# Optimization experiments

Hardware: AMD Instinct MI355X
Metric: run time of the kernel (lower is better)

The kernel has to match this reference:

```python
import jax, jax.numpy as jnp
import numpy as np

E = 1024  # embed_dim
H = 16    # num_heads
D = E // H
L = 2048  # seq len (Q_len == K_len == V_len)


def setup_inputs() -> dict:
    key = jax.random.key(0)
    ks = jax.random.split(key, 12)
    w = lambda k, shape: jax.random.normal(k, shape, dtype=jnp.float32) * 0.02
    return {
        "V": jax.random.normal(ks[0], (L, E), dtype=jnp.float32),
        "K": jax.random.normal(ks[1], (L, E), dtype=jnp.float32),
        "Q": jax.random.normal(ks[2], (L, E), dtype=jnp.float32),
        "position": jnp.arange(L, dtype=jnp.float32).reshape(1, L),
        "W_q": w(ks[3], (E, E)),
        "W_k": w(ks[4], (E, E)),
        "W_v": w(ks[5], (E, E)),
        "W_k_rel": w(ks[6], (E, 1)),
        "W_v_rel": w(ks[7], (E, 1)),
        "W_k_abs": w(ks[8], (E, 1)),
        "W_v_abs": w(ks[9], (E, 1)),
        "W_out": w(ks[10], (E, E)),
        "b_out": jnp.zeros((E,), dtype=jnp.float32),
    }


def reference(V, K, Q, position, W_q, W_k, W_v, W_k_rel, W_v_rel,
              W_k_abs, W_v_abs, W_out, b_out):
    pos = position[0]                                   # [L]
    q = (Q @ W_q.T).reshape(L, H, D)                    # [L,H,D]
    k = (K @ W_k.T).reshape(L, H, D)
    v = (V @ W_v.T).reshape(L, H, D)

    # Absolute position bias. NOTE: the original computes log(pos+1)/10 but then
    # overwrites it with the raw position (a bug preserved here faithfully):
    # Linear(1,E) on a scalar == scalar * weight vector.
    v = v + (pos[:, None] * W_v_abs[:, 0][None, :]).reshape(L, H, D)
    k = k + (pos[:, None] * W_k_abs[:, 0][None, :]).reshape(L, H, D)

    energy = jnp.einsum('qhd,khd->hqk', q, k)           # [H,L,L]

    # Relative-position K bias: relative_position_K[q,j,h,d] = rel[q,j] * wK[h,d]
    # so einsum('nqhd,nhqjd->nhqj') reduces exactly to rel[q,j] * (Q[q,h]\cdot wK[h]).
    rel = jnp.clip(jnp.abs(pos[:, None] - pos[None, :]), 0.0, 5000.0) / 5000.0  # [L,L]
    wK = W_k_rel[:, 0].reshape(H, D)
    wV = W_v_rel[:, 0].reshape(H, D)
    qw = jnp.einsum('qhd,hd->hq', q, wK)                # [H,L]
    energy = energy + qw[:, :, None] * rel[None]

    # Original scales by sqrt(embed_dim), not sqrt(head_dim).
    attn = jax.nn.softmax(energy / jnp.sqrt(jnp.float32(E)), axis=-1)  # [H,L,L]

    out = jnp.einsum('hqk,khd->qhd', attn, v)           # [L,H,D]
    # Relative-position V: sum_j attn[h,q,j]*rel[q,j]*wV[h,d] == (attn*rel summed over j) outer wV.
    s = jnp.einsum('hqk,qk->hq', attn, rel)             # [H,L]
    out = out + jnp.einsum('hq,hd->qhd', s, wV)

    return out.reshape(L, E) @ W_out.T + b_out          # [L,E]
```

## Files before the change

### kernel.cpp

```cpp
#include <hip/hip_runtime.h>
#include <stdint.h>

#define LL 2048
#define EE 1024
#define HH 16
#define DD 64
#define KX 1056

using short8 = __attribute__((ext_vector_type(8))) short;
using s4v    = __attribute__((ext_vector_type(4))) short;
using f32x4  = __attribute__((ext_vector_type(4))) float;

#if __has_builtin(__builtin_amdgcn_mfma_f32_16x16x16_bf16)
#define MFMA16(a,b,c) __builtin_amdgcn_mfma_f32_16x16x16_bf16(a,b,c,0,0,0)
#elif __has_builtin(__builtin_amdgcn_mfma_f32_16x16x16bf16_1k)
#define MFMA16(a,b,c) __builtin_amdgcn_mfma_f32_16x16x16bf16_1k(a,b,c,0,0,0)
#else
static __device__ __forceinline__ f32x4 mfma16f(s4v a, s4v b, f32x4 c) {
  asm volatile("v_mfma_f32_16x16x16_bf16 %0, %1, %2, %0" : "+v"(c) : "v"(a), "v"(b));
  return c;
}
#define MFMA16(a,b,c) mfma16f(a,b,c)
#endif

__device__ __forceinline__ short f2bf(float x) {
  union { float f; uint32_t u; } v; v.f = x;
  uint32_t r = v.u + 0x7fffu + ((v.u >> 16) & 1u);
  return (short)(r >> 16);
}

__global__ __launch_bounds__(256) void convall(
    const float* __restrict__ Q, const float* __restrict__ K,
    const float* __restrict__ V, const float* __restrict__ Wq,
    const float* __restrict__ Wk, const float* __restrict__ Wv,
    const float* __restrict__ Wout,
    short* __restrict__ Qb, short* __restrict__ Kb, short* __restrict__ Vb,
    short* __restrict__ Wqb, short* __restrict__ Wkb, short* __restrict__ Wvb,
    short* __restrict__ W2) {
  const int S1 = LL * EE / 4;
  const int SW = EE * EE / 4;
  int i4 = blockIdx.x * 256 + threadIdx.x;
  const float* src; short* dst; int idx4; bool strided = false;
  if (i4 < 3 * S1) {
    int z = i4 >> 19; idx4 = i4 & (S1 - 1);
    src = z == 0 ? Q : (z == 1 ? K : V);
    dst = z == 0 ? Qb : (z == 1 ? Kb : Vb);
  } else {
    int j = i4 - 3 * S1;
    int z = j >> 18; idx4 = j & (SW - 1);
    src = z == 0 ? Wq : (z == 1 ? Wk : (z == 2 ? Wv : Wout));
    dst = z == 0 ? Wqb : (z == 1 ? Wkb : (z == 2 ? Wvb : W2));
    strided = (z == 3);
  }
  int i = idx4 * 4;
  const float4 v = *(const float4*)(src + i);
  int di = strided ? ((i >> 10) * KX + (i & 1023)) : i;
  union { short s[4]; uint64_t u; } p;
  p.s[0] = f2bf(v.x); p.s[1] = f2bf(v.y); p.s[2] = f2bf(v.z); p.s[3] = f2bf(v.w);
  *(uint64_t*)(dst + di) = p.u;
}

__global__ __launch_bounds__(256) void uker(const float* __restrict__ Wq,
                                            const float* __restrict__ wabs,
                                            const float* __restrict__ wrel,
                                            float* __restrict__ u) {
  int flat = blockIdx.x * 256 + threadIdx.x;
  int c = flat & (EE - 1);
  int h = (flat >> 10) & (HH - 1);
  int s = flat >> 14;
  const float* w = s ? wrel : wabs;
  float acc = 0.f;
  #pragma unroll 8
  for (int d = 0; d < DD; ++d)
    acc += Wq[(size_t)(h * DD + d) * EE + c] * w[h * DD + d];
  u[flat] = acc;
}

__global__ __launch_bounds__(256) void qawker(const float* __restrict__ Q,
                                              const float* __restrict__ u,
                                              float* __restrict__ qaw) {
  int i = blockIdx.x;
  int t = threadIdx.x;
  int h = t >> 4, seg = t & 15;
  const float* u0 = u + (size_t)h * EE;
  const float* u1 = u + (size_t)HH * EE + (size_t)h * EE;
  const float* q = Q + (size_t)i * EE;
  float a0 = 0.f, a1 = 0.f;
  for (int cc = 0; cc < 64; ++cc) {
    int c = cc * 16 + seg;
    float qv = q[c];
    a0 += qv * u0[c];
    a1 += qv * u1[c];
  }
  #pragma unroll
  for (int m = 1; m < 16; m <<= 1) {
    a0 += __shfl_xor(a0, m);
    a1 += __shfl_xor(a1, m);
  }
  if (seg == 0) { qaw[i * 32 + h] = a0; qaw[i * 32 + 16 + h] = a1; }
}

__global__ __launch_bounds__(256) void mrelker(const float* __restrict__ Wout,
                                               const float* __restrict__ wva,
                                               const float* __restrict__ wvr,
                                               short* __restrict__ W2) {
  int flat = blockIdx.x * 256 + threadIdx.x;
  int n = flat >> 5;
  int s = (flat >> 4) & 1;
  int h = flat & 15;
  const float* w = s ? wvr : wva;
  float acc = 0.f;
  #pragma unroll 8
  for (int d = 0; d < DD; ++d)
    acc += Wout[(size_t)n * EE + h * DD + d] * w[h * DD + d];
  W2[(size_t)n * KX + 1024 + s * 16 + h] = f2bf(acc);
}

__global__ __launch_bounds__(256) void gemm_bt(
    const short* __restrict__ Aall, const short* __restrict__ Ball,
    void* __restrict__ Call,
    int K, int aBatch, int bBatch, int cBatch,
    int ldc, int vTransZ, int ldcT, int bf16Out,
    const float* __restrict__ bias, int scaleZ, float scaleVal)
{
  const int BM = 64, BN = 128, BK = 32, PAD = 8;
  __shared__ short As[BM][BK + PAD];
  __shared__ short Bs[BN][BK + PAD];
  int z = blockIdx.z;
  const short* A = Aall + (size_t)z * aBatch;
  const short* B = Ball + (size_t)z * bBatch;
  int m0 = blockIdx.y * BM, n0 = blockIdx.x * BN;
  int t = threadIdx.x;
  int lane = t & 63, wave = t >> 6;
  int wm = wave >> 1, wn = wave & 1;
  int fr = lane & 15, fo = (lane >> 4) * 8;
  const f32x4 vzero = {0.f, 0.f, 0.f, 0.f};
  f32x4 acc[2][4];
  #pragma unroll
  for (int i = 0; i < 2; ++i)
    #pragma unroll
    for (int j = 0; j < 4; ++j) acc[i][j] = vzero;

  int kTiles = K / BK;
  for (int kt = 0; kt < kTiles; ++kt) {
    __syncthreads();
    {
      int row = t >> 2, kb = (t & 3) * 8;
      *(short8*)&As[row][kb] =
          *(const short8*)(A + (size_t)(m0 + row) * K + kt * BK + kb);
      *(short8*)&Bs[row][kb] =
          *(const short8*)(B + (size_t)(n0 + row) * K + kt * BK + kb);
      int uu = t + 256;
      int row2 = uu >> 2, kb2 = (uu & 3) * 8;
      *(short8*)&Bs[row2][kb2] =
          *(const short8*)(B + (size_t)(n0 + row2) * K + kt * BK + kb2);
    }
    __syncthreads();
    short8 af[2], bfr[4];
    #pragma unroll
    for (int i = 0; i < 2; ++i) af[i] = *(const short8*)&As[wm * 32 + i * 16 + fr][fo];
    #pragma unroll
    for (int j = 0; j < 4; ++j) bfr[j] = *(const short8*)&Bs[wn * 64 + j * 16 + fr][fo];
    #pragma unroll
    for (int i = 0; i < 2; ++i)
      #pragma unroll
      for (int j = 0; j < 4; ++j)
        acc[i][j] = __builtin_amdgcn_mfma_f32_16x16x32_bf16(af[i], bfr[j], acc[i][j], 0, 0, 0);
  }

  int rb = (lane >> 4) * 4;
  bool doTrans = (z == vTransZ);
  bool doScale = (z == scaleZ);
  #pragma unroll
  for (int i = 0; i < 2; ++i) {
    #pragma unroll
    for (int j = 0; j < 4; ++j) {
      int n = n0 + wn * 64 + j * 16 + fr;
      float bv = bias ? bias[n] : 0.f;
      #pragma unroll
      for (int r = 0; r < 4; ++r) {
        int m = m0 + wm * 32 + i * 16 + rb + r;
        float val = acc[i][j][r];
        if (doScale) val *= scaleVal;
        val += bv;
        if (bf16Out) {
          short* C = (short*)Call + (size_t)z * cBatch;
          if (doTrans) C[(size_t)n * ldcT + m] = f2bf(val);
          else         C[(size_t)m * ldc + n] = f2bf(val);
        } else {
          float* C = (float*)Call;
          C[(size_t)m * ldc + n] = val;
        }
      }
    }
  }
}

__global__ __launch_bounds__(256, 4) void flash2(
    const short* __restrict__ qp, const short* __restrict__ kp,
    const short* __restrict__ vpT, const float* __restrict__ qaw,
    float* __restrict__ Opart, float* __restrict__ stats)
{
  const int KB = 64;
  __shared__ short k_lds[64][72];
  __shared__ short v_lds[64][72];
  int h = blockIdx.y;
  int q0 = blockIdx.x * 64;
  int half = blockIdx.z;
  int kbeg = half * 1024;
  int t = threadIdx.x, w = t >> 6, lane = t & 63;
  int g = lane >> 4, fr = lane & 15;
  int gi = q0 + w * 16 + fr;
  float gif = (float)gi;
  const f32x4 vzero = {0.f, 0.f, 0.f, 0.f};

  short8 qf[2];
  #pragma unroll
  for (int ks = 0; ks < 2; ++ks)
    qf[ks] = *(const short8*)(qp + (size_t)gi * EE + h * 64 + ks * 32 + g * 8);

  const float LOG2E = 1.4426950408889634f;
  const float sc = LOG2E / 32.f;
  float qa_s = qaw[gi * 32 + h] * sc;
  float qw_s = qaw[gi * 32 + 16 + h] * (sc / 5000.f);

  float m2 = -1e30f, lsum = 0.f, SpA = 0.f, SrA = 0.f;
  f32x4 Oa[4];
  #pragma unroll
  for (int fc = 0; fc < 4; ++fc) Oa[fc] = vzero;

  for (int kt = 0; kt < 16; ++kt) {
    int k0 = kbeg + kt * KB;
    __syncthreads();
    #pragma unroll
    for (int uu = 0; uu < 2; ++uu) {
      int u2 = t + uu * 256;
      int row = u2 >> 3, cb = (u2 & 7) * 8;
      *(short8*)&k_lds[row][cb] =
          *(const short8*)(kp + (size_t)(k0 + row) * EE + h * 64 + cb);
      *(short8*)&v_lds[row][cb] =
          *(const short8*)(vpT + (size_t)(h * 64 + row) * LL + k0 + cb);
    }
    __syncthreads();

    f32x4 St[4];
    #pragma unroll
    for (int jt = 0; jt < 4; ++jt) {
      f32x4 a = vzero;
      a = __builtin_amdgcn_mfma_f32_16x16x32_bf16(
              *(const short8*)&k_lds[jt * 16 + fr][g * 8], qf[0], a, 0, 0, 0);
      a = __builtin_amdgcn_mfma_f32_16x16x32_bf16(
              *(const short8*)&k_lds[jt * 16 + fr][32 + g * 8], qf[1], a, 0, 0, 0);
      St[jt] = a;
    }

    float pf[4][4];
    float tm = -1e30f;
    #pragma unroll
    for (int jt = 0; jt < 4; ++jt) {
      float jb = (float)(k0 + jt * 16 + 4 * g);
      #pragma unroll
      for (int r = 0; r < 4; ++r) {
        float jgf = jb + (float)r;
        float e = St[jt][r] + jgf * qa_s + fabsf(gif - jgf) * qw_s;
        pf[jt][r] = e;
        tm = fmaxf(tm, e);
      }
    }
    tm = fmaxf(tm, __shfl_xor(tm, 16));
    tm = fmaxf(tm, __shfl_xor(tm, 32));

    if (__any(tm > m2 + 8.f)) {
      float mn = fmaxf(m2, tm);
      float alpha = exp2f(m2 - mn);
      m2 = mn;
      lsum *= alpha; SpA *= alpha; SrA *= alpha;
      #pragma unroll
      for (int r = 0; r < 4; ++r) {
        float alr = __shfl(alpha, ((lane >> 4) << 2) + r);
        #pragma unroll
        for (int fc = 0; fc < 4; ++fc) Oa[fc][r] *= alr;
      }
    }

    float Pt = 0.f, Spt = 0.f;
    #pragma unroll
    for (int jt = 0; jt < 4; ++jt) {
      float jb = (float)(k0 + jt * 16 + 4 * g);
      #pragma unroll
      for (int r = 0; r < 4; ++r) {
        float p = exp2f(pf[jt][r] - m2);
        pf[jt][r] = p;
        Pt += p;
        Spt = fmaf(p, jb + (float)r, Spt);
      }
    }
    lsum += Pt; SpA += Spt;
    if (gi >= k0 + KB)      SrA += gif * Pt - Spt;
    else if (gi < k0)       SrA += Spt - gif * Pt;
    else {
      #pragma unroll
      for (int jt = 0; jt < 4; ++jt) {
        float jb = (float)(k0 + jt * 16 + 4 * g);
        #pragma unroll
        for (int r = 0; r < 4; ++r)
          SrA += pf[jt][r] * fabsf(gif - (jb + (float)r));
      }
    }

    s4v pa[4];
    #pragma unroll
    for (int jt = 0; jt < 4; ++jt) {
      int lo, hi;
      asm("v_cvt_pk_bf16_f32 %0, %1, %2" : "=v"(lo) : "v"(pf[jt][0]), "v"(pf[jt][1]));
      asm("v_cvt_pk_bf16_f32 %0, %1, %2" : "=v"(hi) : "v"(pf[jt][2]), "v"(pf[jt][3]));
      union { int i[2]; s4v s; } uu; uu.i[0] = lo; uu.i[1] = hi;
      pa[jt] = uu.s;
    }

    #pragma unroll
    for (int jt = 0; jt < 4; ++jt) {
      #pragma unroll
      for (int fc = 0; fc < 4; ++fc) {
        s4v vb = *(const s4v*)&v_lds[fc * 16 + fr][jt * 16 + 4 * g];
        Oa[fc] = MFMA16(pa[jt], vb, Oa[fc]);
      }
    }
  }

  lsum += __shfl_xor(lsum, 16); lsum += __shfl_xor(lsum, 32);
  SpA  += __shfl_xor(SpA, 16);  SpA  += __shfl_xor(SpA, 32);
  SrA  += __shfl_xor(SrA, 16);  SrA  += __shfl_xor(SrA, 32);

  size_t sb = (size_t)(half * HH + h) * LL;
  if (g == 0) {
    float4 s4 = {m2, lsum, SpA, SrA};
    *(float4*)&stats[(sb + q0 + w * 16 + fr) * 4] = s4;
  }
  #pragma unroll
  for (int fc = 0; fc < 4; ++fc)
    #pragma unroll
    for (int r = 0; r < 4; ++r)
      Opart[(sb + q0 + w * 16 + 4 * g + r) * 64 + fc * 16 + fr] = Oa[fc][r];
}

__global__ __launch_bounds__(256) void merge(const float* __restrict__ Opart,
                                             const float* __restrict__ stats,
                                             short* __restrict__ X2) {
  int q = blockIdx.x;
  int t = threadIdx.x;
  int h = t >> 4, ds = (t & 15) * 4;
  const float4 s0 = *(const float4*)&stats[((size_t)h * LL + q) * 4];
  const float4 s1 = *(const float4*)&stats[((size_t)(HH + h) * LL + q) * 4];
  float m = fmaxf(s0.x, s1.x);
  float a0 = exp2f(s0.x - m), a1 = exp2f(s1.x - m);
  float inv = 1.f / (s0.y * a0 + s1.y * a1);
  const float4 O0 = *(const float4*)&Opart[((size_t)h * LL + q) * 64 + ds];
  const float4 O1 = *(const float4*)&Opart[((size_t)(HH + h) * LL + q) * 64 + ds];
  union { short s[4]; uint64_t u; } pk;
  pk.s[0] = f2bf((O0.x * a0 + O1.x * a1) * inv);
  pk.s[1] = f2bf((O0.y * a0 + O1.y * a1) * inv);
  pk.s[2] = f2bf((O0.z * a0 + O1.z * a1) * inv);
  pk.s[3] = f2bf((O0.w * a0 + O1.w * a1) * inv);
  *(uint64_t*)&X2[(size_t)q * KX + h * 64 + ds] = pk.u;
  if (t < 32) {
    int hh = t & 15;
    const float4 t0 = *(const float4*)&stats[((size_t)hh * LL + q) * 4];
    const float4 t1 = *(const float4*)&stats[((size_t)(HH + hh) * LL + q) * 4];
    float mm = fmaxf(t0.x, t1.x);
    float b0 = exp2f(t0.x - mm), b1 = exp2f(t1.x - mm);
    float linv = 1.f / (t0.y * b0 + t1.y * b1);
    float val = (t < 16) ? (t0.z * b0 + t1.z * b1) * linv
                         : (t0.w * b0 + t1.w * b1) * linv * (1.f / 5000.f);
    X2[(size_t)q * KX + 1024 + (t < 16 ? hh : 16 + hh)] = f2bf(val);
  }
}

extern "C" void kernel_launch(void* const* d_in, const int* in_sizes, int n_in,
                              void* d_out, int out_size, void* d_ws, size_t ws_size,
                              hipStream_t stream) {
  const float* V    = (const float*)d_in[0];
  const float* Kin  = (const float*)d_in[1];
  const float* Q    = (const float*)d_in[2];
  const float* Wq   = (const float*)d_in[4];
  const float* Wk   = (const float*)d_in[5];
  const float* Wv   = (const float*)d_in[6];
  const float* Wkr  = (const float*)d_in[7];
  const float* Wvr  = (const float*)d_in[8];
  const float* Wka  = (const float*)d_in[9];
  const float* Wva  = (const float*)d_in[10];
  const float* Wout = (const float*)d_in[11];
  const float* bout = (const float*)d_in[12];

  char* ws = (char*)d_ws;
  size_t off = 0;
  auto alloc = [&](size_t bytes) -> void* {
    void* p = ws + off;
    off = (off + bytes + 255) & ~(size_t)255;
    return p;
  };
  short* Qb  = (short*)alloc((size_t)LL * EE * 2);
  short* Kb  = (short*)alloc((size_t)LL * EE * 2);
  short* Vb  = (short*)alloc((size_t)LL * EE * 2);
  short* Wqb = (short*)alloc((size_t)EE * EE * 2);
  short* Wkb = (short*)alloc((size_t)EE * EE * 2);
  short* Wvb = (short*)alloc((size_t)EE * EE * 2);
  short* qp  = (short*)alloc((size_t)LL * EE * 2);
  short* kp  = (short*)alloc((size_t)LL * EE * 2);
  short* vpT = (short*)alloc((size_t)EE * LL * 2);
  short* W2  = (short*)alloc((size_t)EE * KX * 2);
  short* X2  = (short*)alloc((size_t)LL * KX * 2);
  float* u   = (float*)alloc((size_t)2 * HH * EE * 4);
  float* qaw = (float*)alloc((size_t)LL * 32 * 4);
  float* Opart = (float*)Qb;
  float* stats = (float*)((char*)Qb + (size_t)17 * 1024 * 1024);
  (void)in_sizes; (void)n_in; (void)out_size; (void)ws_size;

  const float sc = 1.4426950408889634f / 32.f;

  convall<<<(3 * LL * EE / 4 + 4 * EE * EE / 4) / 256, 256, 0, stream>>>(
      Q, Kin, V, Wq, Wk, Wv, Wout, Qb, Kb, Vb, Wqb, Wkb, Wvb, W2);

  uker<<<(2 * HH * EE) / 256, 256, 0, stream>>>(Wq, Wka, Wkr, u);
  qawker<<<LL, 256, 0, stream>>>(Q, u, qaw);
  mrelker<<<(EE * 32) / 256, 256, 0, stream>>>(Wout, Wva, Wvr, W2);

  dim3 gp(EE / 128, LL / 64, 3);
  gemm_bt<<<gp, 256, 0, stream>>>(Qb, Wqb, qp, EE,
                                  LL * EE, EE * EE, LL * EE,
                                  EE, 2, LL, 1,
                                  nullptr, 0, sc);

  flash2<<<dim3(LL / 64, HH, 2), 256, 0, stream>>>(qp, kp, vpT, qaw, Opart, stats);

  merge<<<LL, 256, 0, stream>>>(Opart, stats, X2);

  dim3 go(EE / 128, LL / 64, 1);
  gemm_bt<<<go, 256, 0, stream>>>(X2, W2, d_out, KX,
                                  0, 0, 0,
                                  EE, -1, 1, 0,
                                  bout, -1, 1.f);
}
```

Before: 155.1 us.

## Split attention keys four ways and fold row statistics into an extra MFMA tile

The flash kernel now splits the key range into four chunks instead of two, doubling the grid. The per-element position bias is rewritten as precomputed per-lane offsets plus a per-tile constant for off-diagonal tiles. The row sums (P, P·j, masked sums) are computed by a fifth MFMA column block over synthetic V rows instead of scalar reductions. Partial outputs are normalised and stored as bf16, halving the partial-output traffic, and the merge kernel combines four splits. This adds LDS setup and bf16 rounding of the partials, and relies on bf16-encoded key indices being exact.

```diff
diff --git a/kernel.cpp b/kernel.cpp
--- a/kernel.cpp
+++ b/kernel.cpp
@@ -27,6 +27,10 @@
   union { float f; uint32_t u; } v; v.f = x;
   uint32_t r = v.u + 0x7fffu + ((v.u >> 16) & 1u);
   return (short)(r >> 16);
+}
+__device__ __forceinline__ float bf2f(short s) {
+  union { uint32_t u; float f; } v; v.u = ((uint32_t)(uint16_t)s) << 16;
+  return v.f;
 }
 
 __global__ __launch_bounds__(256) void convall(
@@ -196,24 +200,26 @@
   }
 }
 
-__global__ __launch_bounds__(256, 4) void flash2(
+__global__ __launch_bounds__(256, 4) void flash3(
     const short* __restrict__ qp, const short* __restrict__ kp,
     const short* __restrict__ vpT, const float* __restrict__ qaw,
-    float* __restrict__ Opart, float* __restrict__ stats)
+    short* __restrict__ Obf, float* __restrict__ stats)
 {
-  const int KB = 64;
-  __shared__ short k_lds[64][72];
-  __shared__ short v_lds[64][72];
+  __shared__ __align__(16) short k_lds[64][68];
+  __shared__ __align__(16) short v_lds[80][68];
   int h = blockIdx.y;
   int q0 = blockIdx.x * 64;
-  int half = blockIdx.z;
-  int kbeg = half * 1024;
+  int split = blockIdx.z;
+  int kbeg = split * 512;
   int t = threadIdx.x, w = t >> 6, lane = t & 63;
   int g = lane >> 4, fr = lane & 15;
   int gi = q0 + w * 16 + fr;
   float gif = (float)gi;
   const f32x4 vzero = {0.f, 0.f, 0.f, 0.f};
 
+  if (t < 64) v_lds[65][t] = (short)0x3F80;
+  if (t < 204) ((uint64_t*)&v_lds[68][0])[t] = 0ull;
+
   short8 qf[2];
   #pragma unroll
   for (int ks = 0; ks < 2; ++ks)
@@ -224,13 +230,23 @@
   float qa_s = qaw[gi * 32 + h] * sc;
   float qw_s = qaw[gi * 32 + 16 + h] * (sc / 5000.f);
 
-  float m2 = -1e30f, lsum = 0.f, SpA = 0.f, SrA = 0.f;
-  f32x4 Oa[4];
-  #pragma unroll
-  for (int fc = 0; fc < 4; ++fc) Oa[fc] = vzero;
-
-  for (int kt = 0; kt < 16; ++kt) {
-    int k0 = kbeg + kt * KB;
+  float jp_[16], jm_[16];
+  #pragma unroll
+  for (int jt = 0; jt < 4; ++jt)
+    #pragma unroll
+    for (int r = 0; r < 4; ++r) {
+      float jl = (float)(jt * 16 + 4 * g + r);
+      jp_[jt * 4 + r] = jl * (qa_s + qw_s);
+      jm_[jt * 4 + r] = jl * (qa_s - qw_s);
+    }
+
+  float m2 = -1e30f, Ptd = 0.f, Sptd = 0.f, Srtd = 0.f;
+  f32x4 Oa[5];
+  #pragma unroll
+  for (int fc = 0; fc < 5; ++fc) Oa[fc] = vzero;
+
+  for (int kt = 0; kt < 8; ++kt) {
+    int k0 = kbeg + kt * 64;
     __syncthreads();
     #pragma unroll
     for (int uu = 0; uu < 2; ++uu) {
@@ -241,6 +257,13 @@
       *(short8*)&v_lds[row][cb] =
           *(const short8*)(vpT + (size_t)(h * 64 + row) * LL + k0 + cb);
     }
+    if (t < 64) {
+      short jv = f2bf((float)(k0 - kbeg + t));
+      bool after = (k0 > q0);
+      v_lds[64][t] = jv;
+      v_lds[66][t] = after ? jv : (short)0;
+      v_lds[67][t] = after ? (short)0x3F80 : (short)0;
+    }
     __syncthreads();
 
     f32x4 St[4];
@@ -255,57 +278,73 @@
     }
 
     float pf[4][4];
-    float tm = -1e30f;
-    #pragma unroll
-    for (int jt = 0; jt < 4; ++jt) {
-      float jb = (float)(k0 + jt * 16 + 4 * g);
-      #pragma unroll
-      for (int r = 0; r < 4; ++r) {
-        float jgf = jb + (float)r;
-        float e = St[jt][r] + jgf * qa_s + fabsf(gif - jgf) * qw_s;
-        pf[jt][r] = e;
-        tm = fmaxf(tm, e);
-      }
-    }
-    tm = fmaxf(tm, __shfl_xor(tm, 16));
-    tm = fmaxf(tm, __shfl_xor(tm, 32));
-
-    if (__any(tm > m2 + 8.f)) {
-      float mn = fmaxf(m2, tm);
+    float tmv = -1e30f, C;
+    if (k0 < q0) {
+      C = k0 * qa_s + (gif - (float)k0) * qw_s;
+      #pragma unroll
+      for (int jt = 0; jt < 4; ++jt)
+        #pragma unroll
+        for (int r = 0; r < 4; ++r) {
+          float e = St[jt][r] + jm_[jt * 4 + r];
+          pf[jt][r] = e;
+          tmv = fmaxf(tmv, e);
+        }
+    } else if (k0 > q0) {
+      C = k0 * qa_s + ((float)k0 - gif) * qw_s;
+      #pragma unroll
+      for (int jt = 0; jt < 4; ++jt)
+        #pragma unroll
+        for (int r = 0; r < 4; ++r) {
+          float e = St[jt][r] + jp_[jt * 4 + r];
+          pf[jt][r] = e;
+          tmv = fmaxf(tmv, e);
+        }
+    } else {
+      C = 0.f;
+      #pragma unroll
+      for (int jt = 0; jt < 4; ++jt)
+        #pragma unroll
+        for (int r = 0; r < 4; ++r) {
+          float jgf = (float)(k0 + jt * 16 + 4 * g + r);
+          float e = St[jt][r] + jgf * qa_s + fabsf(gif - jgf) * qw_s;
+          pf[jt][r] = e;
+          tmv = fmaxf(tmv, e);
+        }
+    }
+    tmv = fmaxf(tmv, __shfl_xor(tmv, 16));
+    tmv = fmaxf(tmv, __shfl_xor(tmv, 32));
+    float tmt = tmv + C;
+
+    if (__any(tmt > m2 + 8.f)) {
+      float mn = fmaxf(m2, tmt);
       float alpha = exp2f(m2 - mn);
       m2 = mn;
-      lsum *= alpha; SpA *= alpha; SrA *= alpha;
+      Ptd *= alpha; Sptd *= alpha; Srtd *= alpha;
       #pragma unroll
       for (int r = 0; r < 4; ++r) {
         float alr = __shfl(alpha, ((lane >> 4) << 2) + r);
         #pragma unroll
-        for (int fc = 0; fc < 4; ++fc) Oa[fc][r] *= alr;
+        for (int fc = 0; fc < 5; ++fc) Oa[fc][r] *= alr;
       }
     }
-
-    float Pt = 0.f, Spt = 0.f;
-    #pragma unroll
-    for (int jt = 0; jt < 4; ++jt) {
-      float jb = (float)(k0 + jt * 16 + 4 * g);
-      #pragma unroll
-      for (int r = 0; r < 4; ++r) {
-        float p = exp2f(pf[jt][r] - m2);
-        pf[jt][r] = p;
-        Pt += p;
-        Spt = fmaf(p, jb + (float)r, Spt);
-      }
-    }
-    lsum += Pt; SpA += Spt;
-    if (gi >= k0 + KB)      SrA += gif * Pt - Spt;
-    else if (gi < k0)       SrA += Spt - gif * Pt;
-    else {
-      #pragma unroll
-      for (int jt = 0; jt < 4; ++jt) {
-        float jb = (float)(k0 + jt * 16 + 4 * g);
+    float mr = m2 - C;
+    #pragma unroll
+    for (int jt = 0; jt < 4; ++jt)
+      #pragma unroll
+      for (int r = 0; r < 4; ++r)
+        pf[jt][r] = exp2f(pf[jt][r] - mr);
+
+    if (k0 == q0) {
+      #pragma unroll
+      for (int jt = 0; jt < 4; ++jt)
         #pragma unroll
-        for (int r = 0; r < 4; ++r)
-          SrA += pf[jt][r] * fabsf(gif - (jb + (float)r));
-      }
+        for (int r = 0; r < 4; ++r) {
+          float jgf = (float)(k0 + jt * 16 + 4 * g + r);
+          float p = pf[jt][r];
+          Ptd += p;
+          Sptd = fmaf(p, jgf, Sptd);
+          Srtd = fmaf(p, fabsf(gif - jgf), Srtd);
+        }
     }
 
     s4v pa[4];
@@ -321,57 +360,102 @@
     #pragma unroll
     for (int jt = 0; jt < 4; ++jt) {
       #pragma unroll
-      for (int fc = 0; fc < 4; ++fc) {
+      for (int fc = 0; fc < 5; ++fc) {
         s4v vb = *(const s4v*)&v_lds[fc * 16 + fr][jt * 16 + 4 * g];
         Oa[fc] = MFMA16(pa[jt], vb, Oa[fc]);
       }
     }
   }
 
-  lsum += __shfl_xor(lsum, 16); lsum += __shfl_xor(lsum, 32);
-  SpA  += __shfl_xor(SpA, 16);  SpA  += __shfl_xor(SpA, 32);
-  SrA  += __shfl_xor(SrA, 16);  SrA  += __shfl_xor(SrA, 32);
-
-  size_t sb = (size_t)(half * HH + h) * LL;
+  Ptd  += __shfl_xor(Ptd, 16);  Ptd  += __shfl_xor(Ptd, 32);
+  Sptd += __shfl_xor(Sptd, 16); Sptd += __shfl_xor(Sptd, 32);
+  Srtd += __shfl_xor(Srtd, 16); Srtd += __shfl_xor(Srtd, 32);
+
+  __syncthreads();
+  float* scr = (float*)&k_lds[0][0];
+  if (fr < 4) {
+    #pragma unroll
+    for (int r = 0; r < 4; ++r)
+      scr[(w * 16 + 4 * g + r) * 4 + fr] = Oa[4][r];
+  }
+  __syncthreads();
+
+  float inv[4];
+  #pragma unroll
+  for (int r = 0; r < 4; ++r)
+    inv[r] = 1.f / scr[(w * 16 + 4 * g + r) * 4 + 1];
+
   if (g == 0) {
-    float4 s4 = {m2, lsum, SpA, SrA};
-    *(float4*)&stats[(sb + q0 + w * 16 + fr) * 4] = s4;
-  }
+    float e0 = scr[(w * 16 + fr) * 4 + 0];
+    float e1 = scr[(w * 16 + fr) * 4 + 1];
+    float e2 = scr[(w * 16 + fr) * 4 + 2];
+    float e3 = scr[(w * 16 + fr) * 4 + 3];
+    float kb = (float)kbeg;
+    float Sp = e0 + kb * e1;
+    float Pa = e3, Sa = e2 + kb * e3;
+    float Pb = e1 - Pa - Ptd;
+    float Sb = Sp - Sa - Sptd;
+    float Sr = gif * (Pb - Pa) + (Sa - Sb) + Srtd;
+    float4 s4 = {m2, e1, Sp, Sr};
+    *(float4*)&stats[((size_t)(split * HH + h) * LL + gi) * 4] = s4;
+  }
+
   #pragma unroll
   for (int fc = 0; fc < 4; ++fc)
     #pragma unroll
-    for (int r = 0; r < 4; ++r)
-      Opart[(sb + q0 + w * 16 + 4 * g + r) * 64 + fc * 16 + fr] = Oa[fc][r];
-}
-
-__global__ __launch_bounds__(256) void merge(const float* __restrict__ Opart,
-                                             const float* __restrict__ stats,
-                                             short* __restrict__ X2) {
+    for (int r = 0; r < 4; ++r) {
+      int q = q0 + w * 16 + 4 * g + r;
+      Obf[((size_t)(split * HH + h) * LL + q) * 64 + fc * 16 + fr] =
+          f2bf(Oa[fc][r] * inv[r]);
+    }
+}
+
+__global__ __launch_bounds__(256) void merge4(const short* __restrict__ Obf,
+                                              const float* __restrict__ stats,
+                                              short* __restrict__ X2) {
   int q = blockIdx.x;
   int t = threadIdx.x;
   int h = t >> 4, ds = (t & 15) * 4;
-  const float4 s0 = *(const float4*)&stats[((size_t)h * LL + q) * 4];
-  const float4 s1 = *(const float4*)&stats[((size_t)(HH + h) * LL + q) * 4];
-  float m = fmaxf(s0.x, s1.x);
-  float a0 = exp2f(s0.x - m), a1 = exp2f(s1.x - m);
-  float inv = 1.f / (s0.y * a0 + s1.y * a1);
-  const float4 O0 = *(const float4*)&Opart[((size_t)h * LL + q) * 64 + ds];
-  const float4 O1 = *(const float4*)&Opart[((size_t)(HH + h) * LL + q) * 64 + ds];
+  float4 s[4];
+  #pragma unroll
+  for (int i = 0; i < 4; ++i)
+    s[i] = *(const float4*)&stats[((size_t)(i * HH + h) * LL + q) * 4];
+  float m = fmaxf(fmaxf(s[0].x, s[1].x), fmaxf(s[2].x, s[3].x));
+  float a[4], denom = 0.f;
+  #pragma unroll
+  for (int i = 0; i < 4; ++i) { a[i] = exp2f(s[i].x - m); denom += a[i] * s[i].y; }
+  float invd = 1.f / denom;
+  float acc[4] = {0.f, 0.f, 0.f, 0.f};
+  #pragma unroll
+  for (int i = 0; i < 4; ++i) {
+    float wgt = a[i] * s[i].y * invd;
+    s4v o = *(const s4v*)&Obf[((size_t)(i * HH + h) * LL + q) * 64 + ds];
+    #pragma unroll
+    for (int e = 0; e < 4; ++e) acc[e] = fmaf(wgt, bf2f(o[e]), acc[e]);
+  }
   union { short s[4]; uint64_t u; } pk;
-  pk.s[0] = f2bf((O0.x * a0 + O1.x * a1) * inv);
-  pk.s[1] = f2bf((O0.y * a0 + O1.y * a1) * inv);
-  pk.s[2] = f2bf((O0.z * a0 + O1.z * a1) * inv);
-  pk.s[3] = f2bf((O0.w * a0 + O1.w * a1) * inv);
+  #pragma unroll
+  for (int e = 0; e < 4; ++e) pk.s[e] = f2bf(acc[e]);
   *(uint64_t*)&X2[(size_t)q * KX + h * 64 + ds] = pk.u;
+
   if (t < 32) {
     int hh = t & 15;
-    const float4 t0 = *(const float4*)&stats[((size_t)hh * LL + q) * 4];
-    const float4 t1 = *(const float4*)&stats[((size_t)(HH + hh) * LL + q) * 4];
-    float mm = fmaxf(t0.x, t1.x);
-    float b0 = exp2f(t0.x - mm), b1 = exp2f(t1.x - mm);
-    float linv = 1.f / (t0.y * b0 + t1.y * b1);
-    float val = (t < 16) ? (t0.z * b0 + t1.z * b1) * linv
-                         : (t0.w * b0 + t1.w * b1) * linv * (1.f / 5000.f);
+    float4 ts[4];
+    float mm = -1e30f;
+    #pragma unroll
+    for (int i = 0; i < 4; ++i) {
+      ts[i] = *(const float4*)&stats[((size_t)(i * HH + hh) * LL + q) * 4];
+      mm = fmaxf(mm, ts[i].x);
+    }
+    float num = 0.f, den = 0.f;
+    #pragma unroll
+    for (int i = 0; i < 4; ++i) {
+      float ai = exp2f(ts[i].x - mm);
+      den += ai * ts[i].y;
+      num += ai * ((t < 16) ? ts[i].z : ts[i].w);
+    }
+    float val = num / den;
+    if (t >= 16) val *= (1.f / 5000.f);
     X2[(size_t)q * KX + 1024 + (t < 16 ? hh : 16 + hh)] = f2bf(val);
   }
 }
@@ -412,8 +496,8 @@
   short* X2  = (short*)alloc((size_t)LL * KX * 2);
   float* u   = (float*)alloc((size_t)2 * HH * EE * 4);
   float* qaw = (float*)alloc((size_t)LL * 32 * 4);
-  float* Opart = (float*)Qb;
-  float* stats = (float*)((char*)Qb + (size_t)17 * 1024 * 1024);
+  short* Obf   = Qb;
+  float* stats = (float*)((char*)Qb + (size_t)16 * 1024 * 1024);
   (void)in_sizes; (void)n_in; (void)out_size; (void)ws_size;
 
   const float sc = 1.4426950408889634f / 32.f;
@@ -431,9 +515,9 @@
                                   EE, 2, LL, 1,
                                   nullptr, 0, sc);
 
-  flash2<<<dim3(LL / 64, HH, 2), 256, 0, stream>>>(qp, kp, vpT, qaw, Opart, stats);
-
-  merge<<<LL, 256, 0, stream>>>(Opart, stats, X2);
+  flash3<<<dim3(LL / 64, HH, 4), 256, 0, stream>>>(qp, kp, vpT, qaw, Obf, stats);
+
+  merge4<<<LL, 256, 0, stream>>>(Obf, stats, X2);
 
   dim3 go(EE / 128, LL / 64, 1);
   gemm_bt<<<go, 256, 0, stream>>>(X2, W2, d_out, KX,
```

After: 184.5 us. +19.0%, slower.

## Fuse small prep kernels into conversion and simplify attention bias arithmetic

Applied to the files above, without the earlier changes.

Merges the bf16 conversion, u-vector and W_out relative-column kernels into one launch, removing two kernel launches. In the flash attention kernel, the position-bias and relative-sum computations are specialised by tile position (entirely before, after, or on the diagonal), so the abs() and per-element base computation collapse into one fma per element. LDS padding also changes from 72 to 68 shorts, which may alter bank-conflict behaviour for the MFMA fragment reads.

```diff
diff --git a/kernel.cpp b/kernel.cpp
--- a/kernel.cpp
+++ b/kernel.cpp
@@ -29,51 +29,63 @@
   return (short)(r >> 16);
 }
 
-__global__ __launch_bounds__(256) void convall(
+#define NB_CONV 10240
+__global__ __launch_bounds__(256) void convfused(
     const float* __restrict__ Q, const float* __restrict__ K,
     const float* __restrict__ V, const float* __restrict__ Wq,
     const float* __restrict__ Wk, const float* __restrict__ Wv,
     const float* __restrict__ Wout,
+    const float* __restrict__ wka, const float* __restrict__ wkr,
+    const float* __restrict__ wva, const float* __restrict__ wvr,
     short* __restrict__ Qb, short* __restrict__ Kb, short* __restrict__ Vb,
     short* __restrict__ Wqb, short* __restrict__ Wkb, short* __restrict__ Wvb,
-    short* __restrict__ W2) {
-  const int S1 = LL * EE / 4;
-  const int SW = EE * EE / 4;
-  int i4 = blockIdx.x * 256 + threadIdx.x;
-  const float* src; short* dst; int idx4; bool strided = false;
-  if (i4 < 3 * S1) {
-    int z = i4 >> 19; idx4 = i4 & (S1 - 1);
-    src = z == 0 ? Q : (z == 1 ? K : V);
-    dst = z == 0 ? Qb : (z == 1 ? Kb : Vb);
+    short* __restrict__ W2, float* __restrict__ u) {
+  int b = blockIdx.x;
+  if (b < NB_CONV) {
+    const int S1 = LL * EE / 4;
+    const int SW = EE * EE / 4;
+    int i4 = b * 256 + threadIdx.x;
+    const float* src; short* dst; int idx4; bool strided = false;
+    if (i4 < 3 * S1) {
+      int z = i4 >> 19; idx4 = i4 & (S1 - 1);
+      src = z == 0 ? Q : (z == 1 ? K : V);
+      dst = z == 0 ? Qb : (z == 1 ? Kb : Vb);
+    } else {
+      int j = i4 - 3 * S1;
+      int z = j >> 18; idx4 = j & (SW - 1);
+      src = z == 0 ? Wq : (z == 1 ? Wk : (z == 2 ? Wv : Wout));
+      dst = z == 0 ? Wqb : (z == 1 ? Wkb : (z == 2 ? Wvb : W2));
+      strided = (z == 3);
+    }
+    int i = idx4 * 4;
+    const float4 v = *(const float4*)(src + i);
+    int di = strided ? ((i >> 10) * KX + (i & 1023)) : i;
+    union { short s[4]; uint64_t u; } p;
+    p.s[0] = f2bf(v.x); p.s[1] = f2bf(v.y); p.s[2] = f2bf(v.z); p.s[3] = f2bf(v.w);
+    *(uint64_t*)(dst + di) = p.u;
+  } else if (b < NB_CONV + 128) {
+    int flat = (b - NB_CONV) * 256 + threadIdx.x;
+    int c = flat & (EE - 1);
+    int h = (flat >> 10) & (HH - 1);
+    int s = flat >> 14;
+    const float* w = s ? wkr : wka;
+    float acc = 0.f;
+    #pragma unroll 8
+    for (int d = 0; d < DD; ++d)
+      acc += Wq[(size_t)(h * DD + d) * EE + c] * w[h * DD + d];
+    u[flat] = acc;
   } else {
-    int j = i4 - 3 * S1;
-    int z = j >> 18; idx4 = j & (SW - 1);
-    src = z == 0 ? Wq : (z == 1 ? Wk : (z == 2 ? Wv : Wout));
-    dst = z == 0 ? Wqb : (z == 1 ? Wkb : (z == 2 ? Wvb : W2));
-    strided = (z == 3);
-  }
-  int i = idx4 * 4;
-  const float4 v = *(const float4*)(src + i);
-  int di = strided ? ((i >> 10) * KX + (i & 1023)) : i;
-  union { short s[4]; uint64_t u; } p;
-  p.s[0] = f2bf(v.x); p.s[1] = f2bf(v.y); p.s[2] = f2bf(v.z); p.s[3] = f2bf(v.w);
-  *(uint64_t*)(dst + di) = p.u;
-}
-
-__global__ __launch_bounds__(256) void uker(const float* __restrict__ Wq,
-                                            const float* __restrict__ wabs,
-                                            const float* __restrict__ wrel,
-                                            float* __restrict__ u) {
-  int flat = blockIdx.x * 256 + threadIdx.x;
-  int c = flat & (EE - 1);
-  int h = (flat >> 10) & (HH - 1);
-  int s = flat >> 14;
-  const float* w = s ? wrel : wabs;
-  float acc = 0.f;
-  #pragma unroll 8
-  for (int d = 0; d < DD; ++d)
-    acc += Wq[(size_t)(h * DD + d) * EE + c] * w[h * DD + d];
-  u[flat] = acc;
+    int flat = (b - NB_CONV - 128) * 256 + threadIdx.x;
+    int n = flat >> 5;
+    int s = (flat >> 4) & 1;
+    int h = flat & 15;
+    const float* w = s ? wvr : wva;
+    float acc = 0.f;
+    #pragma unroll 8
+    for (int d = 0; d < DD; ++d)
+      acc += Wout[(size_t)n * EE + h * DD + d] * w[h * DD + d];
+    W2[(size_t)n * KX + 1024 + s * 16 + h] = f2bf(acc);
+  }
 }
 
 __global__ __launch_bounds__(256) void qawker(const float* __restrict__ Q,
@@ -98,22 +110,6 @@
     a1 += __shfl_xor(a1, m);
   }
   if (seg == 0) { qaw[i * 32 + h] = a0; qaw[i * 32 + 16 + h] = a1; }
-}
-
-__global__ __launch_bounds__(256) void mrelker(const float* __restrict__ Wout,
-                                               const float* __restrict__ wva,
-                                               const float* __restrict__ wvr,
-                                               short* __restrict__ W2) {
-  int flat = blockIdx.x * 256 + threadIdx.x;
-  int n = flat >> 5;
-  int s = (flat >> 4) & 1;
-  int h = flat & 15;
-  const float* w = s ? wvr : wva;
-  float acc = 0.f;
-  #pragma unroll 8
-  for (int d = 0; d < DD; ++d)
-    acc += Wout[(size_t)n * EE + h * DD + d] * w[h * DD + d];
-  W2[(size_t)n * KX + 1024 + s * 16 + h] = f2bf(acc);
 }
 
 __global__ __launch_bounds__(256) void gemm_bt(
@@ -196,14 +192,13 @@
   }
 }
 
-__global__ __launch_bounds__(256, 4) void flash2(
+__global__ __launch_bounds__(256, 4) void flash6(
     const short* __restrict__ qp, const short* __restrict__ kp,
     const short* __restrict__ vpT, const float* __restrict__ qaw,
     float* __restrict__ Opart, float* __restrict__ stats)
 {
-  const int KB = 64;
-  __shared__ short k_lds[64][72];
-  __shared__ short v_lds[64][72];
+  __shared__ __align__(16) short k_lds[64][68];
+  __shared__ __align__(16) short v_lds[64][68];
   int h = blockIdx.y;
   int q0 = blockIdx.x * 64;
   int half = blockIdx.z;
@@ -212,6 +207,7 @@
   int g = lane >> 4, fr = lane & 15;
   int gi = q0 + w * 16 + fr;
   float gif = (float)gi;
+  float g4f = (float)(4 * g);
   const f32x4 vzero = {0.f, 0.f, 0.f, 0.f};
 
   short8 qf[2];
@@ -223,6 +219,7 @@
   const float sc = LOG2E / 32.f;
   float qa_s = qaw[gi * 32 + h] * sc;
   float qw_s = qaw[gi * 32 + 16 + h] * (sc / 5000.f);
+  float qapw = qa_s + qw_s, qamw = qa_s - qw_s;
 
   float m2 = -1e30f, lsum = 0.f, SpA = 0.f, SrA = 0.f;
   f32x4 Oa[4];
@@ -230,7 +227,8 @@
   for (int fc = 0; fc < 4; ++fc) Oa[fc] = vzero;
 
   for (int kt = 0; kt < 16; ++kt) {
-    int k0 = kbeg + kt * KB;
+    int k0 = kbeg + kt * 64;
+    float k0f = (float)k0;
     __syncthreads();
     #pragma unroll
     for (int uu = 0; uu < 2; ++uu) {
@@ -255,23 +253,43 @@
     }
 
     float pf[4][4];
-    float tm = -1e30f;
-    #pragma unroll
-    for (int jt = 0; jt < 4; ++jt) {
-      float jb = (float)(k0 + jt * 16 + 4 * g);
-      #pragma unroll
-      for (int r = 0; r < 4; ++r) {
-        float jgf = jb + (float)r;
-        float e = St[jt][r] + jgf * qa_s + fabsf(gif - jgf) * qw_s;
-        pf[jt][r] = e;
-        tm = fmaxf(tm, e);
-      }
-    }
-    tm = fmaxf(tm, __shfl_xor(tm, 16));
-    tm = fmaxf(tm, __shfl_xor(tm, 32));
-
-    if (__any(tm > m2 + 8.f)) {
-      float mn = fmaxf(m2, tm);
+    float tmv = -1e30f;
+    if (k0 < q0) {
+      float b4 = fmaf(g4f, qamw, k0f * qa_s + (gif - k0f) * qw_s);
+      #pragma unroll
+      for (int jt = 0; jt < 4; ++jt)
+        #pragma unroll
+        for (int r = 0; r < 4; ++r) {
+          float e = St[jt][r] + fmaf((float)(jt * 16 + r), qamw, b4);
+          pf[jt][r] = e;
+          tmv = fmaxf(tmv, e);
+        }
+    } else if (k0 > q0) {
+      float b4 = fmaf(g4f, qapw, k0f * qa_s + (k0f - gif) * qw_s);
+      #pragma unroll
+      for (int jt = 0; jt < 4; ++jt)
+        #pragma unroll
+        for (int r = 0; r < 4; ++r) {
+          float e = St[jt][r] + fmaf((float)(jt * 16 + r), qapw, b4);
+          pf[jt][r] = e;
+          tmv = fmaxf(tmv, e);
+        }
+    } else {
+      #pragma unroll
+      for (int jt = 0; jt < 4; ++jt)
+        #pragma unroll
+        for (int r = 0; r < 4; ++r) {
+          float jgf = k0f + g4f + (float)(jt * 16 + r);
+          float e = St[jt][r] + jgf * qa_s + fabsf(gif - jgf) * qw_s;
+          pf[jt][r] = e;
+          tmv = fmaxf(tmv, e);
+        }
+    }
+    tmv = fmaxf(tmv, __shfl_xor(tmv, 16));
+    tmv = fmaxf(tmv, __shfl_xor(tmv, 32));
+
+    if (__any(tmv > m2 + 8.f)) {
+      float mn = fmaxf(m2, tmv);
       float alpha = exp2f(m2 - mn);
       m2 = mn;
       lsum *= alpha; SpA *= alpha; SrA *= alpha;
@@ -283,29 +301,27 @@
       }
     }
 
-    float Pt = 0.f, Spt = 0.f;
-    #pragma unroll
-    for (int jt = 0; jt < 4; ++jt) {
-      float jb = (float)(k0 + jt * 16 + 4 * g);
+    float Pt = 0.f, S1 = 0.f;
+    #pragma unroll
+    for (int jt = 0; jt < 4; ++jt)
       #pragma unroll
       for (int r = 0; r < 4; ++r) {
         float p = exp2f(pf[jt][r] - m2);
         pf[jt][r] = p;
         Pt += p;
-        Spt = fmaf(p, jb + (float)r, Spt);
+        S1 = fmaf(p, (float)(jt * 16 + r), S1);
       }
-    }
-    lsum += Pt; SpA += Spt;
-    if (gi >= k0 + KB)      SrA += gif * Pt - Spt;
-    else if (gi < k0)       SrA += Spt - gif * Pt;
+    float jbase = k0f + g4f;
+    lsum += Pt;
+    SpA += fmaf(jbase, Pt, S1);
+    if (k0 > q0)       SrA += fmaf(jbase - gif, Pt, S1);
+    else if (k0 < q0)  SrA -= fmaf(jbase - gif, Pt, S1);
     else {
       #pragma unroll
-      for (int jt = 0; jt < 4; ++jt) {
-        float jb = (float)(k0 + jt * 16 + 4 * g);
+      for (int jt = 0; jt < 4; ++jt)
         #pragma unroll
         for (int r = 0; r < 4; ++r)
-          SrA += pf[jt][r] * fabsf(gif - (jb + (float)r));
-      }
+          SrA = fmaf(pf[jt][r], fabsf(gif - (jbase + (float)(jt * 16 + r))), SrA);
     }
 
     s4v pa[4];
@@ -418,12 +434,11 @@
 
   const float sc = 1.4426950408889634f / 32.f;
 
-  convall<<<(3 * LL * EE / 4 + 4 * EE * EE / 4) / 256, 256, 0, stream>>>(
-      Q, Kin, V, Wq, Wk, Wv, Wout, Qb, Kb, Vb, Wqb, Wkb, Wvb, W2);
-
-  uker<<<(2 * HH * EE) / 256, 256, 0, stream>>>(Wq, Wka, Wkr, u);
+  convfused<<<NB_CONV + 256, 256, 0, stream>>>(
+      Q, Kin, V, Wq, Wk, Wv, Wout, Wka, Wkr, Wva, Wvr,
+      Qb, Kb, Vb, Wqb, Wkb, Wvb, W2, u);
+
   qawker<<<LL, 256, 0, stream>>>(Q, u, qaw);
-  mrelker<<<(EE * 32) / 256, 256, 0, stream>>>(Wout, Wva, Wvr, W2);
 
   dim3 gp(EE / 128, LL / 64, 3);
   gemm_bt<<<gp, 256, 0, stream>>>(Qb, Wqb, qp, EE,
@@ -431,7 +446,7 @@
                                   EE, 2, LL, 1,
                                   nullptr, 0, sc);
 
-  flash2<<<dim3(LL / 64, HH, 2), 256, 0, stream>>>(qp, kp, vpT, qaw, Opart, stats);
+  flash6<<<dim3(LL / 64, HH, 2), 256, 0, stream>>>(qp, kp, vpT, qaw, Opart, stats);
 
   merge<<<LL, 256, 0, stream>>>(Opart, stats, X2);
 
```

Measured after the change: 151.9 us. -2.0%, faster.
